# Kernel tuning notes

Hardware: AMD Instinct MI355X
Metric: run time of the kernel (lower is better)

## Reference

```python
import jax, jax.numpy as jnp
import numpy as np

D_MODEL = 256
N_HEADS = 8
N_LEVELS = 4
N_POINTS = 4
SHAPES = np.array([[64, 64], [32, 32], [16, 16], [8, 8]], dtype=np.int32)


def setup_inputs() -> dict:
    key = jax.random.key(0)
    ks = jax.random.split(key, 10)
    Lq = int((SHAPES[:, 0] * SHAPES[:, 1]).sum())  # 5440
    N, d = 8, D_MODEL
    noff = N_HEADS * N_LEVELS * N_POINTS * 2
    nw = N_HEADS * N_LEVELS * N_POINTS
    s = 1.0 / np.sqrt(d).astype(np.float32)
    inp = {
        'query': jax.random.normal(ks[0], (N, Lq, d), jnp.float32),
        'reference_points': jax.random.uniform(ks[1], (N, Lq, N_LEVELS, 2), jnp.float32),
        'spatial_shapes': jnp.asarray(SHAPES),
        'level_start_index': jnp.asarray(np.concatenate([[0], np.cumsum(SHAPES[:, 0] * SHAPES[:, 1])[:-1]]).astype(np.int32)),
        'W_value': jax.random.normal(ks[2], (d, d), jnp.float32) * s,
        'b_value': jnp.zeros((d,), jnp.float32),
        'W_off': jax.random.normal(ks[3], (d, noff), jnp.float32) * 0.01,
        'b_off': jax.random.uniform(ks[4], (noff,), jnp.float32, minval=-0.5, maxval=0.5),
        'W_attn': jax.random.normal(ks[5], (d, nw), jnp.float32) * s,
        'b_attn': jnp.zeros((nw,), jnp.float32),
        'W_out': jax.random.normal(ks[6], (d, d), jnp.float32) * s,
        'b_out': jnp.zeros((d,), jnp.float32),
    }
    return inp


def _bilinear_sample(val_l, loc_l, H, W):
    # val_l: [N, h, H*W, dh] flattened level feature map
    # loc_l: [N, Lq, h, P, 2] normalized (x, y) in [0, 1]
    # grid_sample semantics, align_corners=False, zero padding
    N, h, HW, dh = val_l.shape
    Lq, P = loc_l.shape[1], loc_l.shape[3]
    x = loc_l[..., 0] * W - 0.5
    y = loc_l[..., 1] * H - 0.5
    x0 = jnp.floor(x)
    y0 = jnp.floor(y)
    wx = (x - x0)[..., None]  # [N, Lq, h, P, 1]
    wy = (y - y0)[..., None]
    x0i = x0.astype(jnp.int32)
    y0i = y0.astype(jnp.int32)

    def gather(yi, xi):
        valid = (xi >= 0) & (xi < W) & (yi >= 0) & (yi < H)  # [N, Lq, h, P]
        idx = jnp.clip(yi, 0, H - 1) * W + jnp.clip(xi, 0, W - 1)
        idx = idx.transpose(0, 2, 1, 3).reshape(N, h, Lq * P)  # [N, h, Lq*P]
        g = jnp.take_along_axis(val_l, jnp.broadcast_to(idx[..., None], (N, h, Lq * P, dh)), axis=2)
        g = g.reshape(N, h, Lq, P, dh)
        mask = valid.transpose(0, 2, 1, 3)[..., None].astype(val_l.dtype)
        return g * mask

    v00 = gather(y0i, x0i)
    v01 = gather(y0i, x0i + 1)
    v10 = gather(y0i + 1, x0i)
    v11 = gather(y0i + 1, x0i + 1)
    wxt = wx.transpose(0, 2, 1, 3, 4)  # [N, h, Lq, P, 1]
    wyt = wy.transpose(0, 2, 1, 3, 4)
    return (v00 * (1 - wxt) * (1 - wyt) + v01 * wxt * (1 - wyt)
            + v10 * (1 - wxt) * wyt + v11 * wxt * wyt)  # [N, h, Lq, P, dh]


def reference(query, reference_points, spatial_shapes, level_start_index,
              W_value, b_value, W_off, b_off, W_attn, b_attn, W_out, b_out):
    shapes = np.asarray(spatial_shapes)  # static level shapes
    N, Lq, d = query.shape
    h, L, P = N_HEADS, N_LEVELS, N_POINTS
    dh = d // h

    v = query @ W_value + b_value  # value_proj (source reassigns query = value_proj(query))
    off = (v @ W_off + b_off).reshape(N, Lq, h, L, P, 2)
    aw = jax.nn.softmax((v @ W_attn + b_attn).reshape(N, Lq, h, L * P), axis=-1)
    aw = aw.reshape(N, Lq, h, L, P)

    # offset_normalizer = [W_l, H_l]
    norm = jnp.asarray(np.stack([shapes[:, 1], shapes[:, 0]], -1), dtype=v.dtype)  # [L, 2]
    loc = reference_points[:, :, None, :, None, :] + off / norm[None, None, None, :, None, :]

    val = v.reshape(N, Lq, h, dh).transpose(0, 2, 1, 3)  # [N, h, Lv, dh]
    out = jnp.zeros((N, h, Lq, dh), v.dtype)
    start = 0
    for l in range(L):
        H, W = int(shapes[l, 0]), int(shapes[l, 1])
        val_l = val[:, :, start:start + H * W]
        sampled = _bilinear_sample(val_l, loc[:, :, :, l], H, W)  # [N, h, Lq, P, dh]
        w_l = aw[:, :, :, l].transpose(0, 2, 1, 3)[..., None]  # [N, h, Lq, P, 1]
        out = out + (sampled * w_l).sum(axis=3)
        start += H * W

    out = out.transpose(0, 2, 1, 3).reshape(N, Lq, d)
    return out @ W_out + b_out
```

## Files before the change

kernel.cpp:

```cpp
#include <hip/hip_runtime.h>
#include <hip/hip_bf16.h>
#include <cstdint>
#include <cstddef>

#define NB 8
#define LQ 5440
#define MROWS (NB * LQ)

typedef __attribute__((ext_vector_type(8))) _Float16       f16x8;
typedef __attribute__((ext_vector_type(4))) float          f32x4;
typedef __attribute__((ext_vector_type(8))) unsigned short ushort8_t;

__device__ __forceinline__ unsigned short f2h(float f) {
    _Float16 h = (_Float16)f;
    unsigned short u;
    __builtin_memcpy(&u, &h, 2);
    return u;
}
__device__ __forceinline__ float h2f(unsigned short u) {
    _Float16 h;
    __builtin_memcpy(&h, &u, 2);
    return (float)h;
}

__device__ __forceinline__ void xcd_tile(int& bx, int& by) {
    const int nx   = gridDim.x;
    const int nwg  = nx * gridDim.y;
    const int orig = blockIdx.y * nx + blockIdx.x;
    const int q = nwg >> 3, r = nwg & 7;
    const int xcd = orig & 7, pos = orig >> 3;
    const int nw = (xcd < r ? xcd * (q + 1) : r * (q + 1) + (xcd - r) * q) + pos;
    bx = nw % nx;
    by = nw / nx;
}

__global__ __launch_bounds__(256) void prep_weights(
    const float* __restrict__ Wv, const float* __restrict__ Woff,
    const float* __restrict__ Wat, const float* __restrict__ Wo,
    unsigned short* __restrict__ bigBt,
    unsigned short* __restrict__ Wv16n,
    unsigned short* __restrict__ WoaT,
    unsigned short* __restrict__ WoT)
{
    const int id = blockIdx.x * 256 + threadIdx.x;
    if (id < 65536) {
        const int n = id >> 8, k = id & 255;
        bigBt[id] = f2h(Wv[k * 256 + n]);
    } else if (id < 131072) {
        const int p = id - 65536;
        Wv16n[p] = f2h(Wv[p]);
    } else if (id < 131072 + 98304) {
        const int p = id - 131072;
        const int n = p >> 8, k = p & 255;
        WoaT[p] = (n < 256) ? f2h(Woff[k * 256 + n])
                            : f2h(Wat[k * 128 + (n - 256)]);
    } else {
        const int p = id - (131072 + 98304);
        const int n = p >> 8, k = p & 255;
        WoT[p] = f2h(Wo[k * 256 + n]);
    }
}

__global__ __launch_bounds__(256) void combine_bias(
    const float* __restrict__ b_value, const float* __restrict__ Woff,
    const float* __restrict__ Wat, const float* __restrict__ b_off,
    const float* __restrict__ b_attn,
    float* __restrict__ fbias, float* __restrict__ zb)
{
    const int b = blockIdx.x;
    const int t = threadIdx.x;
    if (b < 256) {
        if (t == 0) fbias[b] = b_value[b];
        return;
    }
    if (b >= 640) {
        const int i = (b - 640) * 256 + t;
        if (i < 384) zb[i] = 0.f;
        return;
    }
    const int n = b - 256;
    float p = b_value[t] * ((n < 256) ? Woff[t * 256 + n]
                                      : Wat[t * 128 + (n - 256)]);
    for (int o = 32; o >= 1; o >>= 1) p += __shfl_xor(p, o);
    __shared__ float red[4];
    if ((t & 63) == 0) red[t >> 6] = p;
    __syncthreads();
    if (t == 0) {
        float s = red[0] + red[1] + red[2] + red[3];
        fbias[b] = s + ((n < 256) ? b_off[n] : b_attn[n - 256]);
    }
}

#define LDT 40

template<bool A_FP32, bool F16_OUT>
__global__ __launch_bounds__(256) void gemm_mfma(
    const void* __restrict__ Ap, const unsigned short* __restrict__ Bt,
    const float* __restrict__ bias0, const float* __restrict__ bias1,
    void* __restrict__ C0, void* __restrict__ C1,
    int cs0, int cs1, int split)
{
    __shared__ unsigned short As[128 * LDT];
    __shared__ unsigned short Bs[128 * LDT];

    int bxi, byi;
    xcd_tile(bxi, byi);
    const int bm = byi * 128;
    const int bn = bxi * 128;
    const int t    = threadIdx.x;
    const int lane = t & 63;
    const int wid  = t >> 6;
    const int wm   = (wid >> 1) * 64;
    const int wn   = (wid & 1) * 64;
    const int c    = lane & 15;
    const int qq   = lane >> 4;

    const int tr = t >> 1;
    const int kh = (t & 1) * 16;

    f32x4 acc[4][4];
#pragma unroll
    for (int i = 0; i < 4; ++i)
#pragma unroll
        for (int j = 0; j < 4; ++j)
            acc[i][j] = (f32x4){0.f, 0.f, 0.f, 0.f};

    for (int k0 = 0; k0 < 256; k0 += 32) {
        if (A_FP32) {
            const float4* Af = reinterpret_cast<const float4*>(
                (const float*)Ap + (size_t)(bm + tr) * 256 + k0 + kh);
            const float4 a0 = Af[0], a1 = Af[1], a2 = Af[2], a3 = Af[3];
            ushort8_t u0, u1;
            u0[0]=f2h(a0.x); u0[1]=f2h(a0.y); u0[2]=f2h(a0.z); u0[3]=f2h(a0.w);
            u0[4]=f2h(a1.x); u0[5]=f2h(a1.y); u0[6]=f2h(a1.z); u0[7]=f2h(a1.w);
            u1[0]=f2h(a2.x); u1[1]=f2h(a2.y); u1[2]=f2h(a2.z); u1[3]=f2h(a2.w);
            u1[4]=f2h(a3.x); u1[5]=f2h(a3.y); u1[6]=f2h(a3.z); u1[7]=f2h(a3.w);
            *reinterpret_cast<ushort8_t*>(&As[tr * LDT + kh])     = u0;
            *reinterpret_cast<ushort8_t*>(&As[tr * LDT + kh + 8]) = u1;
        } else {
            const ushort8_t* Ab = reinterpret_cast<const ushort8_t*>(
                (const unsigned short*)Ap + (size_t)(bm + tr) * 256 + k0 + kh);
            *reinterpret_cast<ushort8_t*>(&As[tr * LDT + kh])     = Ab[0];
            *reinterpret_cast<ushort8_t*>(&As[tr * LDT + kh + 8]) = Ab[1];
        }
        {
            const ushort8_t* Bb = reinterpret_cast<const ushort8_t*>(
                Bt + (size_t)(bn + tr) * 256 + k0 + kh);
            *reinterpret_cast<ushort8_t*>(&Bs[tr * LDT + kh])     = Bb[0];
            *reinterpret_cast<ushort8_t*>(&Bs[tr * LDT + kh + 8]) = Bb[1];
        }
        __syncthreads();

        f16x8 af[4], bfr[4];
#pragma unroll
        for (int i = 0; i < 4; ++i)
            af[i] = *reinterpret_cast<const f16x8*>(
                &As[(wm + i * 16 + c) * LDT + qq * 8]);
#pragma unroll
        for (int j = 0; j < 4; ++j)
            bfr[j] = *reinterpret_cast<const f16x8*>(
                &Bs[(wn + j * 16 + c) * LDT + qq * 8]);
#pragma unroll
        for (int i = 0; i < 4; ++i)
#pragma unroll
            for (int j = 0; j < 4; ++j)
                acc[i][j] = __builtin_amdgcn_mfma_f32_16x16x32_f16(
                    af[i], bfr[j], acc[i][j], 0, 0, 0);
        __syncthreads();
    }

#pragma unroll
    for (int j = 0; j < 4; ++j) {
        const int col    = bn + wn + j * 16 + c;
        const bool second = col >= split;
        const int ccol   = second ? col - split : col;
        const float bv   = second ? bias1[ccol] : bias0[ccol];
#pragma unroll
        for (int i = 0; i < 4; ++i) {
#pragma unroll
            for (int r = 0; r < 4; ++r) {
                const int row = bm + wm + i * 16 + qq * 4 + r;
                const float v0 = acc[i][j][r] + bv;
                if (F16_OUT) {
                    const float v1 = __shfl_xor(v0, 1);
                    if ((lane & 1) == 0) {
                        const unsigned int packed =
                            (unsigned int)f2h(v0) | ((unsigned int)f2h(v1) << 16);
                        unsigned short* Cb = (unsigned short*)(second ? C1 : C0);
                        const int cs = second ? cs1 : cs0;
                        *reinterpret_cast<unsigned int*>(
                            Cb + (size_t)row * cs + ccol) = packed;
                    }
                } else {
                    float* Cf = (float*)C0;
                    Cf[(size_t)row * cs0 + col] = v0;
                }
            }
        }
    }
}

__global__ __launch_bounds__(256) void gemm_front(
    const float* __restrict__ Ap, const unsigned short* __restrict__ Bt,
    const float* __restrict__ fbias,
    unsigned short* __restrict__ v16, unsigned short* __restrict__ off16,
    unsigned short* __restrict__ at16)
{
    __shared__ unsigned short As[128 * LDT];
    __shared__ unsigned short Bs[128 * LDT];

    int bxi, byi;
    xcd_tile(bxi, byi);
    const int bm = byi * 128;
    const int bn = bxi * 128;
    const int t    = threadIdx.x;
    const int lane = t & 63;
    const int wid  = t >> 6;
    const int wm   = (wid >> 1) * 64;
    const int wn   = (wid & 1) * 64;
    const int c    = lane & 15;
    const int qq   = lane >> 4;

    const int tr = t >> 1;
    const int kh = (t & 1) * 16;

    f32x4 acc[4][4];
#pragma unroll
    for (int i = 0; i < 4; ++i)
#pragma unroll
        for (int j = 0; j < 4; ++j)
            acc[i][j] = (f32x4){0.f, 0.f, 0.f, 0.f};

    for (int k0 = 0; k0 < 256; k0 += 32) {
        {
            const float4* Af = reinterpret_cast<const float4*>(
                Ap + (size_t)(bm + tr) * 256 + k0 + kh);
            const float4 a0 = Af[0], a1 = Af[1], a2 = Af[2], a3 = Af[3];
            ushort8_t u0, u1;
            u0[0]=f2h(a0.x); u0[1]=f2h(a0.y); u0[2]=f2h(a0.z); u0[3]=f2h(a0.w);
            u0[4]=f2h(a1.x); u0[5]=f2h(a1.y); u0[6]=f2h(a1.z); u0[7]=f2h(a1.w);
            u1[0]=f2h(a2.x); u1[1]=f2h(a2.y); u1[2]=f2h(a2.z); u1[3]=f2h(a2.w);
            u1[4]=f2h(a3.x); u1[5]=f2h(a3.y); u1[6]=f2h(a3.z); u1[7]=f2h(a3.w);
            *reinterpret_cast<ushort8_t*>(&As[tr * LDT + kh])     = u0;
            *reinterpret_cast<ushort8_t*>(&As[tr * LDT + kh + 8]) = u1;
        }
        {
            const ushort8_t* Bb = reinterpret_cast<const ushort8_t*>(
                Bt + (size_t)(bn + tr) * 256 + k0 + kh);
            *reinterpret_cast<ushort8_t*>(&Bs[tr * LDT + kh])     = Bb[0];
            *reinterpret_cast<ushort8_t*>(&Bs[tr * LDT + kh + 8]) = Bb[1];
        }
        __syncthreads();

        f16x8 af[4], bfr[4];
#pragma unroll
        for (int i = 0; i < 4; ++i)
            af[i] = *reinterpret_cast<const f16x8*>(
                &As[(wm + i * 16 + c) * LDT + qq * 8]);
#pragma unroll
        for (int j = 0; j < 4; ++j)
            bfr[j] = *reinterpret_cast<const f16x8*>(
                &Bs[(wn + j * 16 + c) * LDT + qq * 8]);
#pragma unroll
        for (int i = 0; i < 4; ++i)
#pragma unroll
            for (int j = 0; j < 4; ++j)
                acc[i][j] = __builtin_amdgcn_mfma_f32_16x16x32_f16(
                    af[i], bfr[j], acc[i][j], 0, 0, 0);
        __syncthreads();
    }

#pragma unroll
    for (int j = 0; j < 4; ++j) {
        const int col  = bn + wn + j * 16 + c;
        const float bv = fbias[col];
#pragma unroll
        for (int i = 0; i < 4; ++i) {
#pragma unroll
            for (int r = 0; r < 4; ++r) {
                const int row = bm + wm + i * 16 + qq * 4 + r;
                const float v0 = acc[i][j][r] + bv;
                const float v1 = __shfl_xor(v0, 1);
                if ((lane & 1) == 0) {
                    const unsigned int packed =
                        (unsigned int)f2h(v0) | ((unsigned int)f2h(v1) << 16);
                    unsigned short* dst;
                    if (col < 256)      dst = v16   + (size_t)row * 256 + col;
                    else if (col < 512) dst = off16 + (size_t)row * 256 + (col - 256);
                    else                dst = at16  + (size_t)row * 128 + (col - 512);
                    *reinterpret_cast<unsigned int*>(dst) = packed;
                }
            }
        }
    }
}

__global__ __launch_bounds__(256) void sample_kernel(
    const unsigned short* __restrict__ v16,
    const unsigned short* __restrict__ off16,
    const unsigned short* __restrict__ attn16,
    const float* __restrict__ refpts,
    unsigned short* __restrict__ pre16)
{
    const int lane = threadIdx.x & 63;
    const int wv   = threadIdx.x >> 6;
    const int bid  = (blockIdx.x & 7) * 1360 + (blockIdx.x >> 3);
    const int row  = bid * 4 + wv;
    const int n    = row / LQ;

    __shared__ uint4 swi[4][328];

    const ushort4 o4 = reinterpret_cast<const ushort4*>(off16)[(size_t)row * 64 + lane];
    const unsigned int lg = reinterpret_cast<const unsigned int*>(attn16)[(size_t)row * 64 + lane];
    const float l0 = h2f((unsigned short)(lg & 0xffff));
    const float l1 = h2f((unsigned short)(lg >> 16));

    const int h   = lane >> 3;
    const int k   = lane & 7;
    const int lev = k >> 1;
    const float rx = refpts[(size_t)row * 8 + lev * 2 + 0];
    const float ry = refpts[(size_t)row * 8 + lev * 2 + 1];

    float m = fmaxf(l0, l1);
    m = fmaxf(m, __shfl_xor(m, 1));
    m = fmaxf(m, __shfl_xor(m, 2));
    m = fmaxf(m, __shfl_xor(m, 4));
    const float e0 = __expf(l0 - m);
    const float e1 = __expf(l1 - m);
    float s = e0 + e1;
    s += __shfl_xor(s, 1);
    s += __shfl_xor(s, 2);
    s += __shfl_xor(s, 4);
    const float inv = 1.f / s;

    const int  W     = 64 >> lev;
    const int  start = (lev == 0) ? 0 : (lev == 1) ? 4096 : (lev == 2) ? 5120 : 5376;
    const float rs   = 0.015625f * (float)(1 << lev);

#pragma unroll
    for (int pp = 0; pp < 2; ++pp) {
        const float lx = rx + h2f(pp ? o4.z : o4.x) * rs;
        const float ly = ry + h2f(pp ? o4.w : o4.y) * rs;
        const float wgt = (pp ? e1 : e0) * inv;

        const float x = lx * (float)W - 0.5f;
        const float y = ly * (float)W - 0.5f;
        const float fx = floorf(x), fy = floorf(y);
        const int xi = (int)fx, yi = (int)fy;
        const float wx = x - fx, wy = y - fy;

        const int x0 = min(max(xi, 0), W - 1);
        const int x1 = min(max(xi + 1, 0), W - 1);
        const int y0 = min(max(yi, 0), W - 1);
        const int y1 = min(max(yi + 1, 0), W - 1);
        const float vx0 = (xi >= 0 && xi < W)         ? (1.f - wx) : 0.f;
        const float vx1 = (xi + 1 >= 0 && xi + 1 < W) ? wx         : 0.f;
        const float vy0 = (yi >= 0 && yi < W)         ? (1.f - wy) : 0.f;
        const float vy1 = (yi + 1 >= 0 && yi + 1 < W) ? wy         : 0.f;

        const int hb  = h * 64;
        const unsigned int b00 = (unsigned int)((start + y0 * W + x0) * 512 + hb);
        const unsigned int b01 = (unsigned int)((start + y0 * W + x1) * 512 + hb);
        const unsigned int b10 = (unsigned int)((start + y1 * W + x0) * 512 + hb);
        const unsigned int b11 = (unsigned int)((start + y1 * W + x1) * 512 + hb);

        uint4 c0, c1;
        c0.x = __float_as_uint(wgt * vy0 * vx0);
        c0.y = __float_as_uint(wgt * vy0 * vx1);
        c0.z = b00; c0.w = b01;
        c1.x = __float_as_uint(wgt * vy1 * vx0);
        c1.y = __float_as_uint(wgt * vy1 * vx1);
        c1.z = b10; c1.w = b11;
        const int base = h * 41 + 5 * k + 2 * pp;
        swi[wv][base + 0] = c0;
        swi[wv][base + 1] = c1;
    }
    __syncthreads();

    const int cp = (lane >> 2) & 1;
    const int cg = lane & 3;
    const unsigned int koff = cg * 16;

    const int nu = __builtin_amdgcn_readfirstlane(n);
    const char* vn = reinterpret_cast<const char*>(v16) + (size_t)nu * (LQ * 512);
    const uint4* wib = &swi[wv][h * 41 + cp];

#define OFS(j) (2 * (j) + ((j) >> 1))
#define GLD(o) (*reinterpret_cast<const ushort8_t*>(vn + ((o) + koff)))

    float acc[8];
#pragma unroll
    for (int i = 0; i < 8; ++i) acc[i] = 0.f;

    uint4 wi0 = wib[OFS(0)];
    uint4 wi1 = wib[OFS(1)];
    uint4 wi2 = wib[OFS(2)];
    uint4 wi3 = wi2;
    ushort8_t va0 = GLD(wi0.z), vb0 = GLD(wi0.w);
    ushort8_t va1 = GLD(wi1.z), vb1 = GLD(wi1.w);
    ushort8_t va2 = va1,        vb2 = vb1;

#pragma unroll
    for (int j = 0; j < 16; ++j) {
        if (j <= 13) { va2 = GLD(wi2.z); vb2 = GLD(wi2.w); }
        if (j <= 12) wi3 = wib[OFS(j + 3)];

        const float wa = __uint_as_float(wi0.x);
        const float wb = __uint_as_float(wi0.y);
#pragma unroll
        for (int i = 0; i < 8; ++i)
            acc[i] = fmaf(h2f(va0[i]), wa, acc[i]);
#pragma unroll
        for (int i = 0; i < 8; ++i)
            acc[i] = fmaf(h2f(vb0[i]), wb, acc[i]);

        wi0 = wi1; wi1 = wi2; wi2 = wi3;
        va0 = va1; va1 = va2; vb0 = vb1; vb1 = vb2;
    }
#undef OFS
#undef GLD

#pragma unroll
    for (int i = 0; i < 8; ++i)
        acc[i] += __shfl_xor(acc[i], 4);

    if (cp == 0) {
        ushort8_t st;
#pragma unroll
        for (int i = 0; i < 8; ++i) st[i] = f2h(acc[i]);
        *reinterpret_cast<ushort8_t*>(
            pre16 + (size_t)row * 256 + h * 32 + cg * 8) = st;
    }
}

extern "C" void kernel_launch(void* const* d_in, const int* in_sizes, int n_in,
                              void* d_out, int out_size, void* d_ws, size_t ws_size,
                              hipStream_t stream)
{
    const float* query   = (const float*)d_in[0];
    const float* refpts  = (const float*)d_in[1];
    const float* W_value = (const float*)d_in[4];
    const float* b_value = (const float*)d_in[5];
    const float* W_off   = (const float*)d_in[6];
    const float* b_off   = (const float*)d_in[7];
    const float* W_attn  = (const float*)d_in[8];
    const float* b_attn  = (const float*)d_in[9];
    const float* W_out   = (const float*)d_in[10];
    const float* b_out   = (const float*)d_in[11];
    float* out = (float*)d_out;

    unsigned short* ws_v16   = (unsigned short*)d_ws;
    unsigned short* ws_off16 = ws_v16   + (size_t)MROWS * 256;
    unsigned short* ws_at16  = ws_off16 + (size_t)MROWS * 256;
    unsigned short* ws_pre16 = ws_at16  + (size_t)MROWS * 128;
    unsigned short* ws_bigBt = ws_pre16 + (size_t)MROWS * 256;
    unsigned short* ws_wv16n = ws_bigBt + 640 * 256;
    unsigned short* ws_woaT  = ws_wv16n + 65536;
    unsigned short* ws_woT   = ws_woaT  + 98304;
    float*          ws_fbias = (float*)(ws_woT + 65536);
    float*          ws_zb    = ws_fbias + 640;

    prep_weights<<<dim3(1152), 256, 0, stream>>>(
        W_value, W_off, W_attn, W_out, ws_bigBt, ws_wv16n, ws_woaT, ws_woT);

    combine_bias<<<dim3(642), 256, 0, stream>>>(
        b_value, W_off, W_attn, b_off, b_attn, ws_fbias, ws_zb);

    gemm_mfma<false, true><<<dim3(2, 3), 256, 0, stream>>>(
        ws_woaT, ws_wv16n, ws_zb, ws_zb,
        ws_bigBt + 65536, ws_bigBt + 65536, 256, 256, 1 << 30);

    gemm_front<<<dim3(5, 340), 256, 0, stream>>>(
        query, ws_bigBt, ws_fbias, ws_v16, ws_off16, ws_at16);

    sample_kernel<<<dim3(MROWS / 4), 256, 0, stream>>>(
        ws_v16, ws_off16, ws_at16, refpts, ws_pre16);

    gemm_mfma<false, false><<<dim3(2, 340), 256, 0, stream>>>(
        ws_pre16, ws_woT, b_out, b_out, out, out, 256, 256, 1 << 30);
}
```

Before: 146.1 us.

## Use direct global-to-LDS async loads with XOR swizzle; pre-convert query to fp16

Replaces the register-staged tile loads in both GEMM kernels with global_load_lds 16-byte direct copies into an unpadded, XOR-swizzled LDS layout, and fully unrolls the K loop. Because the direct-to-LDS path cannot convert fp32, a separate convert_q16 kernel writes an fp16 copy of the query first, so gemm_front reads fp16 instead of fp32. This is meant to cut VGPR staging traffic and instruction count and to avoid LDS bank conflicts. In exchange it adds an extra kernel launch and a 22 MB write plus re-read of the converted query.

```diff
diff --git a/kernel.cpp b/kernel.cpp
--- a/kernel.cpp
+++ b/kernel.cpp
@@ -21,6 +21,13 @@
     _Float16 h;
     __builtin_memcpy(&h, &u, 2);
     return (float)h;
+}
+
+__device__ __forceinline__ void async16(const void* g, void* l) {
+    __builtin_amdgcn_global_load_lds(
+        (const __attribute__((address_space(1))) void*)g,
+        (__attribute__((address_space(3))) void*)l,
+        16, 0, 0);
 }
 
 __device__ __forceinline__ void xcd_tile(int& bx, int& by) {
@@ -61,6 +68,18 @@
     }
 }
 
+__global__ __launch_bounds__(256) void convert_q16(
+    const float* __restrict__ q, unsigned short* __restrict__ q16)
+{
+    const int idx = blockIdx.x * 256 + threadIdx.x;
+    const float4 a = reinterpret_cast<const float4*>(q)[idx * 2];
+    const float4 b = reinterpret_cast<const float4*>(q)[idx * 2 + 1];
+    ushort8_t u;
+    u[0] = f2h(a.x); u[1] = f2h(a.y); u[2] = f2h(a.z); u[3] = f2h(a.w);
+    u[4] = f2h(b.x); u[5] = f2h(b.y); u[6] = f2h(b.z); u[7] = f2h(b.w);
+    reinterpret_cast<ushort8_t*>(q16)[idx] = u;
+}
+
 __global__ __launch_bounds__(256) void combine_bias(
     const float* __restrict__ b_value, const float* __restrict__ Woff,
     const float* __restrict__ Wat, const float* __restrict__ b_off,
@@ -91,83 +110,83 @@
     }
 }
 
-#define LDT 40
-
-template<bool A_FP32, bool F16_OUT>
+#define GEMM_PRE()                                                            \
+    __shared__ unsigned short As[128 * 32];                                   \
+    __shared__ unsigned short Bs[128 * 32];                                   \
+    int bxi, byi;                                                             \
+    xcd_tile(bxi, byi);                                                       \
+    const int bm = byi * 128;                                                 \
+    const int bn = bxi * 128;                                                 \
+    const int t    = threadIdx.x;                                             \
+    const int lane = t & 63;                                                  \
+    const int wid  = t >> 6;                                                  \
+    const int wm   = (wid >> 1) * 64;                                         \
+    const int wn   = (wid & 1) * 64;                                          \
+    const int c    = lane & 15;                                               \
+    const int qq   = lane >> 4;                                               \
+    const int rA0  = (wid << 5) + (lane >> 2);                                \
+    const int rA1  = rA0 + 16;                                                \
+    const int kqA0 = (lane & 3) ^ ((rA0 >> 1) & 3);                           \
+    const int kqA1 = (lane & 3) ^ ((rA1 >> 1) & 3);                           \
+    const unsigned goffA0 = ((unsigned)(bm + rA0) * 256 + kqA0 * 8) * 2;      \
+    const unsigned goffA1 = ((unsigned)(bm + rA1) * 256 + kqA1 * 8) * 2;      \
+    const unsigned goffB0 = ((unsigned)(bn + rA0) * 256 + kqA0 * 8) * 2;      \
+    const unsigned goffB1 = ((unsigned)(bn + rA1) * 256 + kqA1 * 8) * 2;      \
+    unsigned short* lA0 = As + (wid << 10);                                   \
+    unsigned short* lA1 = lA0 + 512;                                          \
+    unsigned short* lB0 = Bs + (wid << 10);                                   \
+    unsigned short* lB1 = lB0 + 512;                                          \
+    int aoff[4], boff[4];                                                     \
+    _Pragma("unroll")                                                         \
+    for (int i = 0; i < 4; ++i) {                                             \
+        const int ra = wm + i * 16 + c;                                       \
+        aoff[i] = ra * 64 + ((qq ^ ((ra >> 1) & 3)) << 4);                    \
+        const int rb = wn + i * 16 + c;                                       \
+        boff[i] = rb * 64 + ((qq ^ ((rb >> 1) & 3)) << 4);                    \
+    }                                                                         \
+    f32x4 acc[4][4];                                                          \
+    _Pragma("unroll")                                                         \
+    for (int i = 0; i < 4; ++i)                                               \
+        _Pragma("unroll")                                                     \
+        for (int j = 0; j < 4; ++j)                                           \
+            acc[i][j] = (f32x4){0.f, 0.f, 0.f, 0.f};
+
+#define GEMM_KLOOP(Atp, Btp)                                                  \
+    _Pragma("unroll")                                                         \
+    for (int ks = 0; ks < 8; ++ks) {                                          \
+        const unsigned kb = ks * 64;                                          \
+        async16((const char*)(Atp) + goffA0 + kb, lA0);                       \
+        async16((const char*)(Atp) + goffA1 + kb, lA1);                       \
+        async16((const char*)(Btp) + goffB0 + kb, lB0);                       \
+        async16((const char*)(Btp) + goffB1 + kb, lB1);                       \
+        __syncthreads();                                                      \
+        f16x8 af[4], bf[4];                                                   \
+        _Pragma("unroll")                                                     \
+        for (int i = 0; i < 4; ++i)                                           \
+            af[i] = *reinterpret_cast<const f16x8*>(                          \
+                reinterpret_cast<const char*>(As) + aoff[i]);                 \
+        _Pragma("unroll")                                                     \
+        for (int j = 0; j < 4; ++j)                                           \
+            bf[j] = *reinterpret_cast<const f16x8*>(                          \
+                reinterpret_cast<const char*>(Bs) + boff[j]);                 \
+        _Pragma("unroll")                                                     \
+        for (int i = 0; i < 4; ++i)                                           \
+            _Pragma("unroll")                                                 \
+            for (int j = 0; j < 4; ++j)                                       \
+                acc[i][j] = __builtin_amdgcn_mfma_f32_16x16x32_f16(           \
+                    af[i], bf[j], acc[i][j], 0, 0, 0);                        \
+        if (ks < 7) __syncthreads();                                          \
+    }
+
+template<bool F16_OUT>
 __global__ __launch_bounds__(256) void gemm_mfma(
-    const void* __restrict__ Ap, const unsigned short* __restrict__ Bt,
+    const unsigned short* __restrict__ At, const unsigned short* __restrict__ Bt,
     const float* __restrict__ bias0, const float* __restrict__ bias1,
     void* __restrict__ C0, void* __restrict__ C1,
     int cs0, int cs1, int split)
 {
-    __shared__ unsigned short As[128 * LDT];
-    __shared__ unsigned short Bs[128 * LDT];
-
-    int bxi, byi;
-    xcd_tile(bxi, byi);
-    const int bm = byi * 128;
-    const int bn = bxi * 128;
-    const int t    = threadIdx.x;
-    const int lane = t & 63;
-    const int wid  = t >> 6;
-    const int wm   = (wid >> 1) * 64;
-    const int wn   = (wid & 1) * 64;
-    const int c    = lane & 15;
-    const int qq   = lane >> 4;
-
-    const int tr = t >> 1;
-    const int kh = (t & 1) * 16;
-
-    f32x4 acc[4][4];
-#pragma unroll
-    for (int i = 0; i < 4; ++i)
-#pragma unroll
-        for (int j = 0; j < 4; ++j)
-            acc[i][j] = (f32x4){0.f, 0.f, 0.f, 0.f};
-
-    for (int k0 = 0; k0 < 256; k0 += 32) {
-        if (A_FP32) {
-            const float4* Af = reinterpret_cast<const float4*>(
-                (const float*)Ap + (size_t)(bm + tr) * 256 + k0 + kh);
-            const float4 a0 = Af[0], a1 = Af[1], a2 = Af[2], a3 = Af[3];
-            ushort8_t u0, u1;
-            u0[0]=f2h(a0.x); u0[1]=f2h(a0.y); u0[2]=f2h(a0.z); u0[3]=f2h(a0.w);
-            u0[4]=f2h(a1.x); u0[5]=f2h(a1.y); u0[6]=f2h(a1.z); u0[7]=f2h(a1.w);
-            u1[0]=f2h(a2.x); u1[1]=f2h(a2.y); u1[2]=f2h(a2.z); u1[3]=f2h(a2.w);
-            u1[4]=f2h(a3.x); u1[5]=f2h(a3.y); u1[6]=f2h(a3.z); u1[7]=f2h(a3.w);
-            *reinterpret_cast<ushort8_t*>(&As[tr * LDT + kh])     = u0;
-            *reinterpret_cast<ushort8_t*>(&As[tr * LDT + kh + 8]) = u1;
-        } else {
-            const ushort8_t* Ab = reinterpret_cast<const ushort8_t*>(
-                (const unsigned short*)Ap + (size_t)(bm + tr) * 256 + k0 + kh);
-            *reinterpret_cast<ushort8_t*>(&As[tr * LDT + kh])     = Ab[0];
-            *reinterpret_cast<ushort8_t*>(&As[tr * LDT + kh + 8]) = Ab[1];
-        }
-        {
-            const ushort8_t* Bb = reinterpret_cast<const ushort8_t*>(
-                Bt + (size_t)(bn + tr) * 256 + k0 + kh);
-            *reinterpret_cast<ushort8_t*>(&Bs[tr * LDT + kh])     = Bb[0];
-            *reinterpret_cast<ushort8_t*>(&Bs[tr * LDT + kh + 8]) = Bb[1];
-        }
-        __syncthreads();
-
-        f16x8 af[4], bfr[4];
-#pragma unroll
-        for (int i = 0; i < 4; ++i)
-            af[i] = *reinterpret_cast<const f16x8*>(
-                &As[(wm + i * 16 + c) * LDT + qq * 8]);
-#pragma unroll
-        for (int j = 0; j < 4; ++j)
-            bfr[j] = *reinterpret_cast<const f16x8*>(
-                &Bs[(wn + j * 16 + c) * LDT + qq * 8]);
-#pragma unroll
-        for (int i = 0; i < 4; ++i)
-#pragma unroll
-            for (int j = 0; j < 4; ++j)
-                acc[i][j] = __builtin_amdgcn_mfma_f32_16x16x32_f16(
-                    af[i], bfr[j], acc[i][j], 0, 0, 0);
-        __syncthreads();
-    }
+    GEMM_PRE();
+    GEMM_KLOOP(At, Bt);
 
 #pragma unroll
     for (int j = 0; j < 4; ++j) {
@@ -201,74 +220,13 @@
 }
 
 __global__ __launch_bounds__(256) void gemm_front(
-    const float* __restrict__ Ap, const unsigned short* __restrict__ Bt,
+    const unsigned short* __restrict__ At, const unsigned short* __restrict__ Bt,
     const float* __restrict__ fbias,
     unsigned short* __restrict__ v16, unsigned short* __restrict__ off16,
     unsigned short* __restrict__ at16)
 {
-    __shared__ unsigned short As[128 * LDT];
-    __shared__ unsigned short Bs[128 * LDT];
-
-    int bxi, byi;
-    xcd_tile(bxi, byi);
-    const int bm = byi * 128;
-    const int bn = bxi * 128;
-    const int t    = threadIdx.x;
-    const int lane = t & 63;
-    const int wid  = t >> 6;
-    const int wm   = (wid >> 1) * 64;
-    const int wn   = (wid & 1) * 64;
-    const int c    = lane & 15;
-    const int qq   = lane >> 4;
-
-    const int tr = t >> 1;
-    const int kh = (t & 1) * 16;
-
-    f32x4 acc[4][4];
-#pragma unroll
-    for (int i = 0; i < 4; ++i)
-#pragma unroll
-        for (int j = 0; j < 4; ++j)
-            acc[i][j] = (f32x4){0.f, 0.f, 0.f, 0.f};
-
-    for (int k0 = 0; k0 < 256; k0 += 32) {
-        {
-            const float4* Af = reinterpret_cast<const float4*>(
-                Ap + (size_t)(bm + tr) * 256 + k0 + kh);
-            const float4 a0 = Af[0], a1 = Af[1], a2 = Af[2], a3 = Af[3];
-            ushort8_t u0, u1;
-            u0[0]=f2h(a0.x); u0[1]=f2h(a0.y); u0[2]=f2h(a0.z); u0[3]=f2h(a0.w);
-            u0[4]=f2h(a1.x); u0[5]=f2h(a1.y); u0[6]=f2h(a1.z); u0[7]=f2h(a1.w);
-            u1[0]=f2h(a2.x); u1[1]=f2h(a2.y); u1[2]=f2h(a2.z); u1[3]=f2h(a2.w);
-            u1[4]=f2h(a3.x); u1[5]=f2h(a3.y); u1[6]=f2h(a3.z); u1[7]=f2h(a3.w);
-            *reinterpret_cast<ushort8_t*>(&As[tr * LDT + kh])     = u0;
-            *reinterpret_cast<ushort8_t*>(&As[tr * LDT + kh + 8]) = u1;
-        }
-        {
-            const ushort8_t* Bb = reinterpret_cast<const ushort8_t*>(
-                Bt + (size_t)(bn + tr) * 256 + k0 + kh);
-            *reinterpret_cast<ushort8_t*>(&Bs[tr * LDT + kh])     = Bb[0];
-            *reinterpret_cast<ushort8_t*>(&Bs[tr * LDT + kh + 8]) = Bb[1];
-        }
-        __syncthreads();
-
-        f16x8 af[4], bfr[4];
-#pragma unroll
-        for (int i = 0; i < 4; ++i)
-            af[i] = *reinterpret_cast<const f16x8*>(
-                &As[(wm + i * 16 + c) * LDT + qq * 8]);
-#pragma unroll
-        for (int j = 0; j < 4; ++j)
-            bfr[j] = *reinterpret_cast<const f16x8*>(
-                &Bs[(wn + j * 16 + c) * LDT + qq * 8]);
-#pragma unroll
-        for (int i = 0; i < 4; ++i)
-#pragma unroll
-            for (int j = 0; j < 4; ++j)
-                acc[i][j] = __builtin_amdgcn_mfma_f32_16x16x32_f16(
-                    af[i], bfr[j], acc[i][j], 0, 0, 0);
-        __syncthreads();
-    }
+    GEMM_PRE();
+    GEMM_KLOOP(At, Bt);
 
 #pragma unroll
     for (int j = 0; j < 4; ++j) {
@@ -453,7 +411,8 @@
     unsigned short* ws_off16 = ws_v16   + (size_t)MROWS * 256;
     unsigned short* ws_at16  = ws_off16 + (size_t)MROWS * 256;
     unsigned short* ws_pre16 = ws_at16  + (size_t)MROWS * 128;
-    unsigned short* ws_bigBt = ws_pre16 + (size_t)MROWS * 256;
+    unsigned short* ws_q16   = ws_pre16 + (size_t)MROWS * 256;
+    unsigned short* ws_bigBt = ws_q16   + (size_t)MROWS * 256;
     unsigned short* ws_wv16n = ws_bigBt + 640 * 256;
     unsigned short* ws_woaT  = ws_wv16n + 65536;
     unsigned short* ws_woT   = ws_woaT  + 98304;
@@ -466,16 +425,18 @@
     combine_bias<<<dim3(642), 256, 0, stream>>>(
         b_value, W_off, W_attn, b_off, b_attn, ws_fbias, ws_zb);
 
-    gemm_mfma<false, true><<<dim3(2, 3), 256, 0, stream>>>(
+    convert_q16<<<dim3(5440), 256, 0, stream>>>(query, ws_q16);
+
+    gemm_mfma<true><<<dim3(2, 3), 256, 0, stream>>>(
         ws_woaT, ws_wv16n, ws_zb, ws_zb,
         ws_bigBt + 65536, ws_bigBt + 65536, 256, 256, 1 << 30);
 
     gemm_front<<<dim3(5, 340), 256, 0, stream>>>(
-        query, ws_bigBt, ws_fbias, ws_v16, ws_off16, ws_at16);
+        ws_q16, ws_bigBt, ws_fbias, ws_v16, ws_off16, ws_at16);
 
     sample_kernel<<<dim3(MROWS / 4), 256, 0, stream>>>(
         ws_v16, ws_off16, ws_at16, refpts, ws_pre16);
 
-    gemm_mfma<false, false><<<dim3(2, 340), 256, 0, stream>>>(
+    gemm_mfma<false><<<dim3(2, 340), 256, 0, stream>>>(
         ws_pre16, ws_woT, b_out, b_out, out, out, 256, 256, 1 << 30);
 }
```

New measurement: 147.7 us. About the same (+1.1%).
